# Performance work log

Measured on AMD Instinct MI355X. Metric: run time of the kernel, lower is better.

## Reference

```python
import jax, jax.numpy as jnp
import numpy as np

MARGIN = 0.7
EPS = 1e-8  # torch F.cosine_similarity eps


def setup_inputs() -> dict:
    key = jax.random.key(0)
    k1, k2, k3 = jax.random.split(key, 3)
    N, D, C = 4096, 512, 1000
    all_embs = jax.random.normal(k1, (N, D), dtype=jnp.float32)
    labels = jax.random.randint(k2, (N,), 0, C, dtype=jnp.int64)
    Aij = jax.random.uniform(k3, (C, C), dtype=jnp.float32)
    return {"all_embs": all_embs, "labels": labels, "Aij": Aij}


def reference(all_embs, labels, Aij):
    norm = jnp.linalg.norm(all_embs, axis=-1, keepdims=True)
    x = all_embs / jnp.maximum(norm, EPS)              # [N, D]
    sim = x @ x.T                                       # [N, N] cosine sim
    d_emb = 1.0 - sim                                   # pairwise embedding distance
    d_cls = Aij[labels[:, None], labels[None, :]]       # [N, N] gathered class distance
    sigma = ((d_cls < MARGIN) & (d_emb < MARGIN)).astype(jnp.float32)
    loss = jnp.mean(sigma * jnp.square(d_emb - d_cls))
    return loss
```

## Files before the change

### kernel.cpp

```cpp
#include <hip/hip_runtime.h>
#include <hip/hip_fp8.h>

#define NN 4096
#define DD 512
#define CC 1000
#define NB 64

typedef __attribute__((ext_vector_type(4))) float f32x4;

__global__ __launch_bounds__(256) void knorm(const float* __restrict__ embs,
                                             unsigned char* __restrict__ Xq,
                                             float* __restrict__ out) {
  int tid = threadIdx.x;
  if (blockIdx.x == 0 && tid == 0) out[0] = 0.f;
  int lane = tid & 63;
  int row = blockIdx.x * 4 + (tid >> 6);
  const float* rp = embs + (size_t)row * DD;
  float4 v0 = ((const float4*)rp)[lane * 2];
  float4 v1 = ((const float4*)rp)[lane * 2 + 1];
  float ss = v0.x * v0.x + v0.y * v0.y + v0.z * v0.z + v0.w * v0.w +
             v1.x * v1.x + v1.y * v1.y + v1.z * v1.z + v1.w * v1.w;
  for (int off = 32; off; off >>= 1) ss += __shfl_xor(ss, off);
  float scale = 1.0f / fmaxf(sqrtf(ss), 1e-8f);
  float f[8] = {v0.x, v0.y, v0.z, v0.w, v1.x, v1.y, v1.z, v1.w};
  unsigned long long o = 0;
#pragma unroll
  for (int i = 0; i < 8; ++i) {
    __hip_fp8_e4m3 q(f[i] * scale);
    o |= (unsigned long long)q.__x << (8 * i);
  }
  *(unsigned long long*)(Xq + (size_t)row * DD + lane * 8) = o;
}

__global__ __launch_bounds__(256) void kmain(const unsigned char* __restrict__ Xq,
                                             const int* __restrict__ labels,
                                             const float* __restrict__ Aij,
                                             float* __restrict__ out) {
  __shared__ __align__(16) unsigned char As[64 * 128];
  __shared__ __align__(16) unsigned char Bs[64 * 128];
  int tid = threadIdx.x;
  int lane = tid & 63;
  int w = tid >> 6;
  int wr = w >> 1, wc = w & 1;

  int t = blockIdx.x;
  int by = 0;
  while (t >= (NB - by)) { t -= (NB - by); ++by; }
  int bx = by + t;
  int row0 = by * 64;
  int col0 = bx * 64;

  f32x4 acc[2][2];
#pragma unroll
  for (int m = 0; m < 2; ++m)
#pragma unroll
    for (int n = 0; n < 2; ++n) acc[m][n] = (f32x4){0.f, 0.f, 0.f, 0.f};

  for (int it = 0; it < DD / 128; ++it) {
    int k0 = it * 128;
    if (it) __syncthreads();
#pragma unroll
    for (int i = 0; i < 2; ++i) {
      int idx = i * 256 + tid;
      int r = idx >> 3;
      int c = idx & 7;
      int srcB = ((c ^ (r & 7)) << 4);
      const unsigned char* ga = Xq + (size_t)(row0 + r) * DD + k0 + srcB;
      const unsigned char* gb = Xq + (size_t)(col0 + r) * DD + k0 + srcB;
      __builtin_amdgcn_global_load_lds(
          (const __attribute__((address_space(1))) void*)ga,
          (__attribute__((address_space(3))) void*)(As + idx * 16), 16, 0, 0);
      __builtin_amdgcn_global_load_lds(
          (const __attribute__((address_space(1))) void*)gb,
          (__attribute__((address_space(3))) void*)(Bs + idx * 16), 16, 0, 0);
    }
    __syncthreads();
#pragma unroll
    for (int ks = 0; ks < 4; ++ks) {
      int q = (ks << 1) | (lane >> 5);
      int o = ((lane >> 4) & 1) << 3;
      long a[2], b[2];
#pragma unroll
      for (int m = 0; m < 2; ++m) {
        int r = wr * 32 + m * 16 + (lane & 15);
        a[m] = *(const long*)(As + r * 128 + (((q ^ (r & 7)) << 4) | o));
      }
#pragma unroll
      for (int n = 0; n < 2; ++n) {
        int r = wc * 32 + n * 16 + (lane & 15);
        b[n] = *(const long*)(Bs + r * 128 + (((q ^ (r & 7)) << 4) | o));
      }
#pragma unroll
      for (int m = 0; m < 2; ++m)
#pragma unroll
        for (int n = 0; n < 2; ++n)
          acc[m][n] = __builtin_amdgcn_mfma_f32_16x16x32_fp8_fp8(a[m], b[n],
                                                                 acc[m][n], 0, 0, 0);
    }
  }

  float lsum = 0.f;
#pragma unroll
  for (int m = 0; m < 2; ++m) {
#pragma unroll
    for (int n = 0; n < 2; ++n) {
#pragma unroll
      for (int j = 0; j < 4; ++j) {
        float s = acc[m][n][j];
        float de = 1.0f - s;
        if (de < 0.7f) {
          int row = row0 + wr * 32 + m * 16 + ((lane >> 4) * 4 + j);
          int col = col0 + wc * 32 + n * 16 + (lane & 15);
          if (col >= row) {
            int lr = labels[row], lc = labels[col];
            float dc = Aij[lr * CC + lc];
            if (dc < 0.7f) {
              float d = de - dc;
              lsum += d * d;
            }
            if (col > row) {
              float dc2 = Aij[lc * CC + lr];
              if (dc2 < 0.7f) {
                float d = de - dc2;
                lsum += d * d;
              }
            }
          }
        }
      }
    }
  }
  for (int off = 32; off; off >>= 1) lsum += __shfl_xor(lsum, off);
  __shared__ float red[4];
  if ((tid & 63) == 0) red[w] = lsum;
  __syncthreads();
  if (tid == 0) {
    float v = (red[0] + red[1] + red[2] + red[3]) * (1.0f / ((float)NN * (float)NN));
    if (v != 0.f) atomicAdd(out, v);
  }
}

extern "C" void kernel_launch(void* const* d_in, const int* in_sizes, int n_in,
                              void* d_out, int out_size, void* d_ws, size_t ws_size,
                              hipStream_t stream) {
  const float* embs = (const float*)d_in[0];
  const int* labels = (const int*)d_in[1];
  const float* Aij = (const float*)d_in[2];
  float* out = (float*)d_out;
  unsigned char* Xq = (unsigned char*)d_ws;

  knorm<<<NN / 4, 256, 0, stream>>>(embs, Xq, out);
  kmain<<<(NB * (NB + 1)) / 2, 256, 0, stream>>>(Xq, labels, Aij, out);
}
```

Before: 24.16 us.

## Use persistent blocks over paired tile rows, loading full K and reusing A tile

Launches 512 persistent blocks in place of one block per upper-triangular tile. Each block processes 4-5 tiles drawn from a pair of complementary tile rows (sr and 63-sr) so every block gets the same amount of work. The full K=512 slice is loaded into LDS in one go, and the A tile is reused while the tile row is unchanged. This cuts block-launch count, K-loop syncs and redundant A loads. LDS per block rises to 64KB, which limits occupancy, and there is no overlap between loads and MFMA within a block.

Measured after the change: 27.40 us. +13.4%, slower.

```diff
diff --git a/kernel.cpp b/kernel.cpp
--- a/kernel.cpp
+++ b/kernel.cpp
@@ -36,59 +36,72 @@
                                              const int* __restrict__ labels,
                                              const float* __restrict__ Aij,
                                              float* __restrict__ out) {
-  __shared__ __align__(16) unsigned char As[64 * 128];
-  __shared__ __align__(16) unsigned char Bs[64 * 128];
+  __shared__ __align__(16) unsigned char As[64 * 512];
+  __shared__ __align__(16) unsigned char Bs[64 * 512];
   int tid = threadIdx.x;
   int lane = tid & 63;
   int w = tid >> 6;
   int wr = w >> 1, wc = w & 1;
 
-  int t = blockIdx.x;
-  int by = 0;
-  while (t >= (NB - by)) { t -= (NB - by); ++by; }
-  int bx = by + t;
-  int row0 = by * 64;
-  int col0 = bx * 64;
+  int sr = blockIdx.x >> 4;
+  int slot = blockIdx.x & 15;
+  int start = slot ? 5 + (slot - 1) * 4 : 0;
+  int cnt = slot ? 4 : 5;
+  int len1 = NB - sr;
 
-  f32x4 acc[2][2];
+  int cur_by = -1;
+  float lsum = 0.f;
+
+  for (int jj = 0; jj < cnt; ++jj) {
+    int j = start + jj;
+    int by, bx;
+    if (j < len1) { by = sr;      bx = sr + j; }
+    else          { by = 63 - sr; bx = 63 - sr + (j - len1); }
+    int row0 = by * 64;
+    int col0 = bx * 64;
+
+    if (jj) __syncthreads();
+    bool loadA = (by != cur_by);
+    cur_by = by;
 #pragma unroll
-  for (int m = 0; m < 2; ++m)
-#pragma unroll
-    for (int n = 0; n < 2; ++n) acc[m][n] = (f32x4){0.f, 0.f, 0.f, 0.f};
-
-  for (int it = 0; it < DD / 128; ++it) {
-    int k0 = it * 128;
-    if (it) __syncthreads();
-#pragma unroll
-    for (int i = 0; i < 2; ++i) {
+    for (int i = 0; i < 8; ++i) {
       int idx = i * 256 + tid;
-      int r = idx >> 3;
-      int c = idx & 7;
+      int r = idx >> 5;
+      int c = idx & 31;
       int srcB = ((c ^ (r & 7)) << 4);
-      const unsigned char* ga = Xq + (size_t)(row0 + r) * DD + k0 + srcB;
-      const unsigned char* gb = Xq + (size_t)(col0 + r) * DD + k0 + srcB;
-      __builtin_amdgcn_global_load_lds(
-          (const __attribute__((address_space(1))) void*)ga,
-          (__attribute__((address_space(3))) void*)(As + idx * 16), 16, 0, 0);
+      if (loadA) {
+        const unsigned char* ga = Xq + (size_t)(row0 + r) * DD + srcB;
+        __builtin_amdgcn_global_load_lds(
+            (const __attribute__((address_space(1))) void*)ga,
+            (__attribute__((address_space(3))) void*)(As + idx * 16), 16, 0, 0);
+      }
+      const unsigned char* gb = Xq + (size_t)(col0 + r) * DD + srcB;
       __builtin_amdgcn_global_load_lds(
           (const __attribute__((address_space(1))) void*)gb,
           (__attribute__((address_space(3))) void*)(Bs + idx * 16), 16, 0, 0);
     }
     __syncthreads();
+
+    f32x4 acc[2][2];
 #pragma unroll
-    for (int ks = 0; ks < 4; ++ks) {
+    for (int m = 0; m < 2; ++m)
+#pragma unroll
+      for (int n = 0; n < 2; ++n) acc[m][n] = (f32x4){0.f, 0.f, 0.f, 0.f};
+
+#pragma unroll
+    for (int ks = 0; ks < 16; ++ks) {
       int q = (ks << 1) | (lane >> 5);
       int o = ((lane >> 4) & 1) << 3;
       long a[2], b[2];
 #pragma unroll
       for (int m = 0; m < 2; ++m) {
         int r = wr * 32 + m * 16 + (lane & 15);
-        a[m] = *(const long*)(As + r * 128 + (((q ^ (r & 7)) << 4) | o));
+        a[m] = *(const long*)(As + r * 512 + (((q ^ (r & 7)) << 4) | o));
       }
 #pragma unroll
       for (int n = 0; n < 2; ++n) {
         int r = wc * 32 + n * 16 + (lane & 15);
-        b[n] = *(const long*)(Bs + r * 128 + (((q ^ (r & 7)) << 4) | o));
+        b[n] = *(const long*)(Bs + r * 512 + (((q ^ (r & 7)) << 4) | o));
       }
 #pragma unroll
       for (int m = 0; m < 2; ++m)
@@ -97,32 +110,31 @@
           acc[m][n] = __builtin_amdgcn_mfma_f32_16x16x32_fp8_fp8(a[m], b[n],
                                                                  acc[m][n], 0, 0, 0);
     }
-  }
 
-  float lsum = 0.f;
 #pragma unroll
-  for (int m = 0; m < 2; ++m) {
+    for (int m = 0; m < 2; ++m) {
 #pragma unroll
-    for (int n = 0; n < 2; ++n) {
+      for (int n = 0; n < 2; ++n) {
 #pragma unroll
-      for (int j = 0; j < 4; ++j) {
-        float s = acc[m][n][j];
-        float de = 1.0f - s;
-        if (de < 0.7f) {
-          int row = row0 + wr * 32 + m * 16 + ((lane >> 4) * 4 + j);
-          int col = col0 + wc * 32 + n * 16 + (lane & 15);
-          if (col >= row) {
-            int lr = labels[row], lc = labels[col];
-            float dc = Aij[lr * CC + lc];
-            if (dc < 0.7f) {
-              float d = de - dc;
-              lsum += d * d;
-            }
-            if (col > row) {
-              float dc2 = Aij[lc * CC + lr];
-              if (dc2 < 0.7f) {
-                float d = de - dc2;
+        for (int jv = 0; jv < 4; ++jv) {
+          float s = acc[m][n][jv];
+          float de = 1.0f - s;
+          if (de < 0.7f) {
+            int row = row0 + wr * 32 + m * 16 + ((lane >> 4) * 4 + jv);
+            int col = col0 + wc * 32 + n * 16 + (lane & 15);
+            if (col >= row) {
+              int lr = labels[row], lc = labels[col];
+              float dc = Aij[lr * CC + lc];
+              if (dc < 0.7f) {
+                float d = de - dc;
                 lsum += d * d;
+              }
+              if (col > row) {
+                float dc2 = Aij[lc * CC + lr];
+                if (dc2 < 0.7f) {
+                  float d = de - dc2;
+                  lsum += d * d;
+                }
               }
             }
           }
@@ -130,6 +142,7 @@
       }
     }
   }
+
   for (int off = 32; off; off >>= 1) lsum += __shfl_xor(lsum, off);
   __shared__ float red[4];
   if ((tid & 63) == 0) red[w] = lsum;
@@ -150,5 +163,5 @@
   unsigned char* Xq = (unsigned char*)d_ws;
 
   knorm<<<NN / 4, 256, 0, stream>>>(embs, Xq, out);
-  kmain<<<(NB * (NB + 1)) / 2, 256, 0, stream>>>(Xq, labels, Aij, out);
+  kmain<<<512, 256, 0, stream>>>(Xq, labels, Aij, out);
 }
```

## Double-buffer LDS tiles to overlap global loads with MFMA compute

Applied to the files above, without the earlier changes.

Adds a second LDS buffer for the A and B tiles and unrolls the four-step K loop into a pipelined sequence. The load for the next K chunk is issued before computing the current one, with explicit vmcnt waits and barriers. This hides global-to-LDS load latency behind MFMA work, at the cost of doubling LDS use per block, which may reduce occupancy. It also relies on hand-written waitcnt counts that must match the number of outstanding loads.

Measured after the change: 26.31 us. 8.9% more time.

```diff
diff --git a/kernel.cpp b/kernel.cpp
--- a/kernel.cpp
+++ b/kernel.cpp
@@ -36,8 +36,8 @@
                                              const int* __restrict__ labels,
                                              const float* __restrict__ Aij,
                                              float* __restrict__ out) {
-  __shared__ __align__(16) unsigned char As[64 * 128];
-  __shared__ __align__(16) unsigned char Bs[64 * 128];
+  __shared__ __align__(16) unsigned char As[2][64 * 128];
+  __shared__ __align__(16) unsigned char Bs[2][64 * 128];
   int tid = threadIdx.x;
   int lane = tid & 63;
   int w = tid >> 6;
@@ -56,48 +56,69 @@
 #pragma unroll
     for (int n = 0; n < 2; ++n) acc[m][n] = (f32x4){0.f, 0.f, 0.f, 0.f};
 
-  for (int it = 0; it < DD / 128; ++it) {
-    int k0 = it * 128;
-    if (it) __syncthreads();
-#pragma unroll
-    for (int i = 0; i < 2; ++i) {
-      int idx = i * 256 + tid;
-      int r = idx >> 3;
-      int c = idx & 7;
-      int srcB = ((c ^ (r & 7)) << 4);
-      const unsigned char* ga = Xq + (size_t)(row0 + r) * DD + k0 + srcB;
-      const unsigned char* gb = Xq + (size_t)(col0 + r) * DD + k0 + srcB;
-      __builtin_amdgcn_global_load_lds(
-          (const __attribute__((address_space(1))) void*)ga,
-          (__attribute__((address_space(3))) void*)(As + idx * 16), 16, 0, 0);
-      __builtin_amdgcn_global_load_lds(
-          (const __attribute__((address_space(1))) void*)gb,
-          (__attribute__((address_space(3))) void*)(Bs + idx * 16), 16, 0, 0);
-    }
-    __syncthreads();
-#pragma unroll
-    for (int ks = 0; ks < 4; ++ks) {
-      int q = (ks << 1) | (lane >> 5);
-      int o = ((lane >> 4) & 1) << 3;
-      long a[2], b[2];
-#pragma unroll
-      for (int m = 0; m < 2; ++m) {
-        int r = wr * 32 + m * 16 + (lane & 15);
-        a[m] = *(const long*)(As + r * 128 + (((q ^ (r & 7)) << 4) | o));
-      }
-#pragma unroll
-      for (int n = 0; n < 2; ++n) {
-        int r = wc * 32 + n * 16 + (lane & 15);
-        b[n] = *(const long*)(Bs + r * 128 + (((q ^ (r & 7)) << 4) | o));
-      }
-#pragma unroll
-      for (int m = 0; m < 2; ++m)
-#pragma unroll
-        for (int n = 0; n < 2; ++n)
-          acc[m][n] = __builtin_amdgcn_mfma_f32_16x16x32_fp8_fp8(a[m], b[n],
-                                                                 acc[m][n], 0, 0, 0);
-    }
+#define STAGE(b, itv)                                                           \
+  {                                                                             \
+    int k0_ = (itv) * 128;                                                      \
+    _Pragma("unroll") for (int i = 0; i < 2; ++i) {                             \
+      int idx = i * 256 + tid;                                                  \
+      int r = idx >> 3;                                                         \
+      int c = idx & 7;                                                          \
+      int srcB = ((c ^ (r & 7)) << 4);                                          \
+      const unsigned char* ga = Xq + (size_t)(row0 + r) * DD + k0_ + srcB;      \
+      const unsigned char* gb = Xq + (size_t)(col0 + r) * DD + k0_ + srcB;      \
+      __builtin_amdgcn_global_load_lds(                                         \
+          (const __attribute__((address_space(1))) void*)ga,                    \
+          (__attribute__((address_space(3))) void*)(As[b] + idx * 16), 16, 0, 0);\
+      __builtin_amdgcn_global_load_lds(                                         \
+          (const __attribute__((address_space(1))) void*)gb,                    \
+          (__attribute__((address_space(3))) void*)(Bs[b] + idx * 16), 16, 0, 0);\
+    }                                                                           \
   }
+
+#define COMPUTE(bf)                                                             \
+  {                                                                             \
+    _Pragma("unroll") for (int ks = 0; ks < 4; ++ks) {                          \
+      int q = (ks << 1) | (lane >> 5);                                          \
+      int o = ((lane >> 4) & 1) << 3;                                           \
+      long a[2], b[2];                                                          \
+      _Pragma("unroll") for (int m = 0; m < 2; ++m) {                           \
+        int r = wr * 32 + m * 16 + (lane & 15);                                 \
+        a[m] = *(const long*)(As[bf] + r * 128 + (((q ^ (r & 7)) << 4) | o));   \
+      }                                                                         \
+      _Pragma("unroll") for (int n = 0; n < 2; ++n) {                           \
+        int r = wc * 32 + n * 16 + (lane & 15);                                 \
+        b[n] = *(const long*)(Bs[bf] + r * 128 + (((q ^ (r & 7)) << 4) | o));   \
+      }                                                                         \
+      _Pragma("unroll") for (int m = 0; m < 2; ++m)                             \
+        _Pragma("unroll") for (int n = 0; n < 2; ++n)                           \
+          acc[m][n] = __builtin_amdgcn_mfma_f32_16x16x32_fp8_fp8(               \
+              a[m], b[n], acc[m][n], 0, 0, 0);                                  \
+    }                                                                           \
+  }
+
+  STAGE(0, 0);
+  STAGE(1, 1);
+  asm volatile("s_waitcnt vmcnt(4)" ::: "memory");
+  __builtin_amdgcn_s_barrier();
+  COMPUTE(0);
+  asm volatile("s_waitcnt lgkmcnt(0)" ::: "memory");
+  __builtin_amdgcn_s_barrier();
+  STAGE(0, 2);
+  asm volatile("s_waitcnt vmcnt(4)" ::: "memory");
+  __builtin_amdgcn_s_barrier();
+  COMPUTE(1);
+  asm volatile("s_waitcnt lgkmcnt(0)" ::: "memory");
+  __builtin_amdgcn_s_barrier();
+  STAGE(1, 3);
+  asm volatile("s_waitcnt vmcnt(4)" ::: "memory");
+  __builtin_amdgcn_s_barrier();
+  COMPUTE(0);
+  asm volatile("s_waitcnt lgkmcnt(0) vmcnt(0)" ::: "memory");
+  __builtin_amdgcn_s_barrier();
+  COMPUTE(1);
+
+#undef STAGE
+#undef COMPUTE
 
   float lsum = 0.f;
 #pragma unroll
@@ -105,11 +126,11 @@
 #pragma unroll
     for (int n = 0; n < 2; ++n) {
 #pragma unroll
-      for (int j = 0; j < 4; ++j) {
-        float s = acc[m][n][j];
+      for (int jv = 0; jv < 4; ++jv) {
+        float s = acc[m][n][jv];
         float de = 1.0f - s;
         if (de < 0.7f) {
-          int row = row0 + wr * 32 + m * 16 + ((lane >> 4) * 4 + j);
+          int row = row0 + wr * 32 + m * 16 + ((lane >> 4) * 4 + jv);
           int col = col0 + wc * 32 + n * 16 + (lane & 15);
           if (col >= row) {
             int lr = labels[row], lc = labels[col];
```
